# Kernel optimization log

Hardware: AMD Instinct MI355X
Metric: run time of the kernel (lower is better)

## Reference

```python
import jax, jax.numpy as jnp
import numpy as np

EPS = 1e-5
HEAD_SPLIT = 16   # MAB_new self.K: torch.split chunk size along channels (= head dim)
NUM_D = 16        # MAB_new self.d: becomes the number of heads; attn scale = 1/sqrt(d)


def _fc(x, W, b, g, be):
    # conv2d_ with 1x1 kernel acting on last dim + BatchNorm2d (training-mode
    # batch statistics over B,T,N per channel) + ReLU.  x: [B,T,N,Cin]
    y = jnp.einsum('btnc,oc->btno', x, W) + b
    mu = y.mean(axis=(0, 1, 2), keepdims=True)
    var = y.var(axis=(0, 1, 2), keepdims=True)  # biased var, as torch BN
    return jax.nn.relu(g * (y - mu) * jax.lax.rsqrt(var + EPS) + be)


def _mab(Q, Kin, pq, pk, pv, po):
    q = _fc(Q, *pq)
    k = _fc(Kin, *pk)
    v = _fc(Kin, *pv)
    B, Sq, N, D = q.shape
    Sk = k.shape[1]
    h = D // HEAD_SPLIT  # = NUM_D heads of size HEAD_SPLIT (split/cat quirk)
    qh = q.reshape(B, Sq, N, h, HEAD_SPLIT)
    kh = k.reshape(B, Sk, N, h, HEAD_SPLIT)
    vh = v.reshape(B, Sk, N, h, HEAD_SPLIT)
    scale = np.float32(1.0 / np.sqrt(NUM_D))
    attn = jnp.einsum('bqnhc,bknhc->bnhqk', qh, kh) * scale
    attn = jax.nn.softmax(attn, axis=-1)
    out = jnp.einsum('bnhqk,bknhc->bqnhc', attn, vh).reshape(B, Sq, N, D)
    return _fc(out, *po)


def _forward(X, TE, SE, I,
             m0qW, m0qb, m0qg, m0qz, m0kW, m0kb, m0kg, m0kz,
             m0vW, m0vb, m0vg, m0vz, m0oW, m0ob, m0og, m0oz,
             m1qW, m1qb, m1qg, m1qz, m1kW, m1kb, m1kg, m1kz,
             m1vW, m1vb, m1vg, m1vz, m1oW, m1ob, m1og, m1oz):
    mid = X
    Xc = jnp.concatenate([X, TE, SE], axis=-1)           # [B,T,N,3D]
    Ir = jnp.broadcast_to(I, (X.shape[0],) + I.shape[1:])  # [B,set_dim,N,3D]
    H = _mab(Ir, Xc, (m0qW, m0qb, m0qg, m0qz), (m0kW, m0kb, m0kg, m0kz),
             (m0vW, m0vb, m0vg, m0vz), (m0oW, m0ob, m0og, m0oz))
    res = _mab(Xc, H, (m1qW, m1qb, m1qg, m1qz), (m1kW, m1kb, m1kg, m1kz),
               (m1vW, m1vb, m1vg, m1vz), (m1oW, m1ob, m1og, m1oz))
    return mid + res


def setup_inputs() -> dict:
    key = jax.random.key(0)
    ks = list(jax.random.split(key, 64))
    B, T, N, D = 16, 12, 500, 256
    DD, S = 3 * D, 32
    nxt = iter(ks)

    def w(o, i):
        return jax.random.normal(next(nxt), (o, i), jnp.float32) * np.float32(1.0 / np.sqrt(i))

    inp = {
        'X': jax.random.normal(next(nxt), (B, T, N, D), jnp.float32),
        'TE': jax.random.normal(next(nxt), (B, T, N, D), jnp.float32),
        'SE': jax.random.normal(next(nxt), (B, T, N, D), jnp.float32),
        'I': jax.random.normal(next(nxt), (1, S, N, DD), jnp.float32) * np.float32(0.02),
    }
    layer_shapes = {'m0': [('q', D, DD), ('k', D, DD), ('v', D, DD), ('o', DD, D)],
                    'm1': [('q', D, DD), ('k', D, DD), ('v', D, DD), ('o', D, D)]}
    for pre in ('m0', 'm1'):
        for name, o, i in layer_shapes[pre]:
            inp[pre + name + 'W'] = w(o, i)
            inp[pre + name + 'b'] = jnp.zeros((o,), jnp.float32)
            inp[pre + name + 'g'] = jax.random.uniform(next(nxt), (o,), jnp.float32, 0.5, 1.5)
            inp[pre + name + 'z'] = jax.random.normal(next(nxt), (o,), jnp.float32) * np.float32(0.1)
    inp['mask'] = jnp.ones((1,), jnp.bool_)  # unused in original forward
    return inp


def reference(X, TE, SE, I,
              m0qW, m0qb, m0qg, m0qz, m0kW, m0kb, m0kg, m0kz,
              m0vW, m0vb, m0vg, m0vz, m0oW, m0ob, m0og, m0oz,
              m1qW, m1qb, m1qg, m1qz, m1kW, m1kb, m1kg, m1kz,
              m1vW, m1vb, m1vg, m1vz, m1oW, m1ob, m1og, m1oz, mask):
    return _forward(X, TE, SE, I,
                    m0qW, m0qb, m0qg, m0qz, m0kW, m0kb, m0kg, m0kz,
                    m0vW, m0vb, m0vg, m0vz, m0oW, m0ob, m0og, m0oz,
                    m1qW, m1qb, m1qg, m1qz, m1kW, m1kb, m1kg, m1kz,
                    m1vW, m1vb, m1vg, m1vz, m1oW, m1ob, m1og, m1oz)
```

## Files before the change

kernel.cpp:

```cpp
#include <hip/hip_runtime.h>
#include <stdint.h>

typedef __bf16 bf16_t;
typedef bf16_t bf16x8 __attribute__((ext_vector_type(8)));
typedef float f32x4 __attribute__((ext_vector_type(4)));

__device__ __forceinline__ float bf2f(unsigned short u) {
  union { unsigned int i; float f; } x; x.i = ((unsigned int)u) << 16; return x.f;
}
__device__ __forceinline__ unsigned short f2bf(float f) {
  union { float f; unsigned int i; } x; x.f = f;
  unsigned int r = x.i + 0x7FFFu + ((x.i >> 16) & 1u);
  return (unsigned short)(r >> 16);
}
__device__ __forceinline__ unsigned pack2(float a, float b) {
  return (unsigned)f2bf(a) | ((unsigned)f2bf(b) << 16);
}

__global__ void cat3(const float* __restrict__ a, const float* __restrict__ b,
                     const float* __restrict__ c, float* __restrict__ dst) {
  int i = threadIdx.x;
  dst[i] = a[i]; dst[256 + i] = b[i]; dst[512 + i] = c[i];
}

__global__ __launch_bounds__(256) void wsplit(
    const float* __restrict__ in, unsigned short* __restrict__ hi,
    unsigned short* __restrict__ lo, int n) {
  int i = (blockIdx.x * 256 + threadIdx.x) * 8;
  if (i >= n) return;
  float4 a = *(const float4*)(in + i);
  float4 b = *(const float4*)(in + i + 4);
  float f[8] = {a.x, a.y, a.z, a.w, b.x, b.y, b.z, b.w};
  unsigned short sh[8], sl[8];
#pragma unroll
  for (int j = 0; j < 8; ++j) {
    sh[j] = f2bf(f[j]);
    sl[j] = f2bf(f[j] - bf2f(sh[j]));
  }
  *(uint4*)(hi + i) = *(uint4*)sh;
  *(uint4*)(lo + i) = *(uint4*)sl;
}

struct f8 { float4 a, b; };

__device__ __forceinline__ f8 ld_c8(const float* __restrict__ X,
                                    const float* __restrict__ TE,
                                    const float* __restrict__ SE,
                                    size_t row, int cc) {
  const float* src = (cc < 256) ? X : ((cc < 512) ? TE : SE);
  const float* p = src + row * 256 + (cc & 255);
  f8 r; r.a = *(const float4*)p; r.b = *(const float4*)(p + 4);
  return r;
}
__device__ __forceinline__ uint4 pack_hi(const float4 a, const float4 b) {
  return make_uint4(pack2(a.x, a.y), pack2(a.z, a.w), pack2(b.x, b.y), pack2(b.z, b.w));
}

template<int AMODE, int SMODE, int PART, int PREC, int K>
__global__ __launch_bounds__(512) void gemm7(
    const void* __restrict__ Ap, const float* __restrict__ AX,
    const float* __restrict__ ATE, const float* __restrict__ ASE,
    const unsigned short* __restrict__ Wh, const unsigned short* __restrict__ Wl,
    const float* __restrict__ bias, const float2* __restrict__ ssO,
    unsigned short* __restrict__ Cb, unsigned short* __restrict__ Cb2,
    float* __restrict__ psum, float* __restrict__ psq,
    int Cout, int cstr, int pOff, int nx) {
  constexpr int ASH = 64 * K;
  constexpr int TOT = ASH + (SMODE != 0 ? 64 * 136 : 8);
  constexpr int NC = K / 128;
  __shared__ unsigned short lds[TOT];
  unsigned short* lA = lds;
  unsigned short* lC = lds + ASH;

  const int tid = threadIdx.x;
  const int lane = tid & 63, wid = tid >> 6;
  const int l15 = lane & 15, l4 = lane >> 4;
  const int brow = blockIdx.x * 64;

  constexpr int CPR = K / 8;
#pragma unroll
  for (int i = 0; i < (64 * CPR) / 512; ++i) {
    int ch = i * 512 + tid;
    int row = ch / CPR, c8 = (ch % CPR) * 8;
    uint4 hv;
    if constexpr (AMODE == 2) {
      hv = *(const uint4*)((const unsigned short*)Ap + (size_t)(brow + row) * K + c8);
    } else if constexpr (AMODE == 0) {
      const float* p = (const float*)Ap + (size_t)(brow + row) * K + c8;
      hv = pack_hi(*(const float4*)p, *(const float4*)(p + 4));
    } else {
      f8 v = ld_c8(AX, ATE, ASE, (size_t)(brow + row), c8);
      hv = pack_hi(v.a, v.b);
    }
    int dst = row * K + (c8 & ~63) + ((c8 & 63) ^ ((row & 7) << 3));
    *(uint4*)(lA + dst) = hv;
  }
  __syncthreads();

  const int axor = (l15 & 7) << 3;
  const int colL = wid * 16 + l15;

  for (int cx = 0; cx < nx; ++cx) {
    const int bcol = cx * 256;
    const bool lo0 = (PREC == 2) || (PREC == 3 && bcol >= 256);
    const bool lo1 = (PREC == 2) || (PREC == 3 && bcol + 128 >= 256);
    const unsigned short* wH0 = Wh + (size_t)(bcol + colL) * K + l4 * 8;
    const unsigned short* wH1 = wH0 + (size_t)128 * K;
    const unsigned short* wL0 = nullptr;
    const unsigned short* wL1 = nullptr;
    if constexpr (PREC >= 2) {
      wL0 = Wl + (size_t)(bcol + colL) * K + l4 * 8;
      wL1 = wL0 + (size_t)128 * K;
    }
    f32x4 acc[4][2] = {};

#pragma unroll
    for (int c = 0; c < NC; ++c) {
      uint4 bh0[4], bh1[4], bl0[4], bl1[4];
#pragma unroll
      for (int ks = 0; ks < 4; ++ks) {
        bh0[ks] = *(const uint4*)(wH0 + c * 128 + ks * 32);
        bh1[ks] = *(const uint4*)(wH1 + c * 128 + ks * 32);
      }
      if constexpr (PREC >= 2) {
        if (lo0) {
#pragma unroll
          for (int ks = 0; ks < 4; ++ks) bl0[ks] = *(const uint4*)(wL0 + c * 128 + ks * 32);
        }
        if (lo1) {
#pragma unroll
          for (int ks = 0; ks < 4; ++ks) bl1[ks] = *(const uint4*)(wL1 + c * 128 + ks * 32);
        }
      }
#pragma unroll
      for (int kk = 0; kk < 4; ++kk) {
        const int kabs = c * 128 + kk * 32;
        const int kt64 = kabs & ~63;
        const int cofs = ((kabs & 32) + l4 * 8) ^ axor;
        bf16x8 af[4];
#pragma unroll
        for (int m = 0; m < 4; ++m)
          af[m] = *(const bf16x8*)(lA + (m * 16 + l15) * K + kt64 + cofs);
        bf16x8 b0 = *(const bf16x8*)&bh0[kk];
        bf16x8 b1 = *(const bf16x8*)&bh1[kk];
#pragma unroll
        for (int m = 0; m < 4; ++m) {
          acc[m][0] = __builtin_amdgcn_mfma_f32_16x16x32_bf16(af[m], b0, acc[m][0], 0, 0, 0);
          acc[m][1] = __builtin_amdgcn_mfma_f32_16x16x32_bf16(af[m], b1, acc[m][1], 0, 0, 0);
        }
        if constexpr (PREC >= 2) {
          if (lo0) {
            bf16x8 c0 = *(const bf16x8*)&bl0[kk];
#pragma unroll
            for (int m = 0; m < 4; ++m)
              acc[m][0] = __builtin_amdgcn_mfma_f32_16x16x32_bf16(af[m], c0, acc[m][0], 0, 0, 0);
          }
          if (lo1) {
            bf16x8 c1 = *(const bf16x8*)&bl1[kk];
#pragma unroll
            for (int m = 0; m < 4; ++m)
              acc[m][1] = __builtin_amdgcn_mfma_f32_16x16x32_bf16(af[m], c1, acc[m][1], 0, 0, 0);
          }
        }
      }
    }

#pragma unroll
    for (int s = 0; s < 2; ++s) {
      const int bcs = bcol + s * 128;
      const int col = bcs + colL;
      float cs = 0.f, cq = 0.f;
      float bv = bias[col];
      float2 s2 = make_float2(1.f, 0.f);
      if constexpr (SMODE == 2) s2 = ssO[col];
      if constexpr (SMODE != 0) __syncthreads();
#pragma unroll
      for (int m = 0; m < 4; ++m) {
#pragma unroll
        for (int r = 0; r < 4; ++r) {
          float v = acc[m][s][r] + bv;
          if constexpr (PART) { cs += v; cq += v * v; }
          if constexpr (SMODE == 2) v = fmaxf(v * s2.x + s2.y, 0.f);
          if constexpr (SMODE != 0) lC[(m * 16 + l4 * 4 + r) * 136 + colL] = f2bf(v);
        }
      }
      if constexpr (SMODE != 0) {
        __syncthreads();
        const int rw = tid >> 4, c16 = (tid & 15) * 8;
#pragma unroll
        for (int it = 0; it < 2; ++it) {
          int rr = it * 32 + rw;
          uint4 val = *(const uint4*)(lC + rr * 136 + c16);
          if constexpr (SMODE == 5) {
            unsigned short* dst = (bcs < 256) ? Cb : Cb2;
            *(uint4*)(dst + (size_t)(brow + rr) * 256 + (bcs & 255) + c16) = val;
          } else if constexpr (SMODE == 6) {
            if (bcs < 512)
              *(uint4*)(Cb + (size_t)(brow + rr) * 512 + bcs + c16) = val;
            else
              *(uint4*)(Cb2 + (size_t)(brow + rr) * 256 + (bcs - 512) + c16) = val;
          } else {
            *(uint4*)(Cb + (size_t)(brow + rr) * cstr + bcs + c16) = val;
          }
        }
      }
      if constexpr (PART) {
        cs += __shfl_xor(cs, 16); cs += __shfl_xor(cs, 32);
        cq += __shfl_xor(cq, 16); cq += __shfl_xor(cq, 32);
        if (l4 == 0) {
          size_t pidx = (size_t)(pOff + blockIdx.x) * Cout + col;
          psum[pidx] = cs;
          psq[pidx]  = cq;
        }
      }
    }
  }
}

__global__ __launch_bounds__(256) void colstats(
    const unsigned short* __restrict__ A, float* __restrict__ psum,
    float* __restrict__ psq) {
  const int tid = threadIdx.x;
  const int r8 = tid >> 5, co = tid & 31;
  float s[8] = {0,0,0,0,0,0,0,0}, q[8] = {0,0,0,0,0,0,0,0};
  size_t base = (size_t)blockIdx.x * 2048;
  for (int it = 0; it < 256; ++it) {
    size_t row = base + it * 8 + r8;
    uint4 v = *(const uint4*)(A + row * 256 + co * 8);
    const unsigned short* pv = (const unsigned short*)&v;
#pragma unroll
    for (int j = 0; j < 8; ++j) {
      float f = bf2f(pv[j]);
      s[j] += f; q[j] += f * f;
    }
  }
  __shared__ float ls[8][32][8], lq[8][32][8];
#pragma unroll
  for (int j = 0; j < 8; ++j) { ls[r8][co][j] = s[j]; lq[r8][co][j] = q[j]; }
  __syncthreads();
  int co2 = tid >> 3, j2 = tid & 7;
  float S = 0.f, Q = 0.f;
#pragma unroll
  for (int r = 0; r < 8; ++r) { S += ls[r][co2][j2]; Q += lq[r][co2][j2]; }
  psum[(size_t)blockIdx.x * 256 + co2 * 8 + j2] = S;
  psq [(size_t)blockIdx.x * 256 + co2 * 8 + j2] = Q;
}

__global__ __launch_bounds__(512) void bn_part(
    const float* __restrict__ psum, const float* __restrict__ psq,
    float* __restrict__ pp, int gridM, int Cout) {
  const int lane = threadIdx.x & 63, wv = threadIdx.x >> 6;
  const int c = blockIdx.y * 64 + lane;
  float s = 0.f, q = 0.f;
  for (int r = blockIdx.x + 64 * wv; r < gridM; r += 512) {
    s += psum[(size_t)r * Cout + c];
    q += psq[(size_t)r * Cout + c];
  }
  __shared__ float rs[8][64], rq[8][64];
  rs[wv][lane] = s; rq[wv][lane] = q;
  __syncthreads();
  if (threadIdx.x < 64) {
    float S = 0.f, Q = 0.f;
#pragma unroll
    for (int w2 = 0; w2 < 8; ++w2) { S += rs[w2][threadIdx.x]; Q += rq[w2][threadIdx.x]; }
    pp[(size_t)blockIdx.x * Cout + blockIdx.y * 64 + threadIdx.x] = S;
    pp[(size_t)(64 + blockIdx.x) * Cout + blockIdx.y * 64 + threadIdx.x] = Q;
  }
}
__global__ __launch_bounds__(64) void bn_fin(
    const float* __restrict__ pp, const float* __restrict__ g,
    const float* __restrict__ be, float2* __restrict__ ss,
    int CoutT, int colOff, float invR) {
  int c = blockIdx.x * 64 + threadIdx.x;
  int cp = colOff + c;
  float S = 0.f, Q = 0.f;
  for (int r = 0; r < 64; ++r) {
    S += pp[(size_t)r * CoutT + cp];
    Q += pp[(size_t)(64 + r) * CoutT + cp];
  }
  float mu = S * invR, var = Q * invR - mu * mu;
  float sc = g[c] * rsqrtf(var + 1e-5f);
  ss[c] = make_float2(sc, be[c] - mu * sc);
}
__global__ __launch_bounds__(64) void bn_fin2(
    const float* __restrict__ pp, const float* __restrict__ gA,
    const float* __restrict__ zA, const float* __restrict__ gB,
    const float* __restrict__ zB, float2* __restrict__ ssC,
    int CoutT, float invR) {
  int c = blockIdx.x * 64 + threadIdx.x;
  float S = 0.f, Q = 0.f;
  for (int r = 0; r < 64; ++r) {
    S += pp[(size_t)r * CoutT + c];
    Q += pp[(size_t)(64 + r) * CoutT + c];
  }
  float mu = S * invR, var = Q * invR - mu * mu;
  const float* g = (c < 256) ? gA : gB;
  const float* z = (c < 256) ? zA : zB;
  int ci = c & 255;
  float sc = g[ci] * rsqrtf(var + 1e-5f);
  ssC[c] = make_float2(sc, z[ci] - mu * sc);
}

template<int NK, int NQ>
__global__ void attn_sm(const unsigned short* __restrict__ qy,
                        const unsigned short* __restrict__ ky,
                        const unsigned short* __restrict__ vy,
                        const float2* __restrict__ ssq, const float2* __restrict__ ssk,
                        const float2* __restrict__ ssv, unsigned short* __restrict__ out,
                        size_t qStride, size_t kvStride, size_t oStride, int RS) {
  __shared__ float kl[NK][16][17];
  __shared__ float vl[NK][16][17];
  const int n = blockIdx.x, b = blockIdx.y;
  const int tid = threadIdx.x;
  const unsigned short* kyb = ky + (size_t)b * kvStride;
  const unsigned short* vyb = vy + (size_t)b * kvStride;
  for (int ch = tid; ch < NK * 32; ch += NQ * 16) {
    int t = ch >> 5, c8 = (ch & 31) * 8;
    size_t src = ((size_t)t * 500 + n) * RS + c8;
    uint4 kv = *(const uint4*)(kyb + src);
    uint4 vv = *(const uint4*)(vyb + src);
    const unsigned short* kp = (const unsigned short*)&kv;
    const unsigned short* vp = (const unsigned short*)&vv;
#pragma unroll
    for (int j = 0; j < 8; ++j) {
      int c = c8 + j;
      float2 sk = ssk[c], sv = ssv[c];
      kl[t][c >> 4][c & 15] = fmaxf(bf2f(kp[j]) * sk.x + sk.y, 0.f);
      vl[t][c >> 4][c & 15] = fmaxf(bf2f(vp[j]) * sv.x + sv.y, 0.f);
    }
  }
  __syncthreads();
  const int s = tid >> 4, h = tid & 15;
  unsigned short qraw[16];
  size_t qb = (size_t)b * qStride + ((size_t)s * 500 + n) * 256 + h * 16;
  *(uint4*)qraw = *(const uint4*)(qy + qb);
  *(uint4*)(qraw + 8) = *(const uint4*)(qy + qb + 8);
  float qv[16];
#pragma unroll
  for (int c = 0; c < 16; ++c) {
    float2 sq = ssq[h * 16 + c];
    qv[c] = fmaxf(bf2f(qraw[c]) * sq.x + sq.y, 0.f);
  }
  float lg[NK], mx = -1e30f;
#pragma unroll
  for (int t = 0; t < NK; ++t) {
    float d = 0.f;
#pragma unroll
    for (int c = 0; c < 16; ++c) d += qv[c] * kl[t][h][c];
    lg[t] = d * 0.25f;
    mx = fmaxf(mx, lg[t]);
  }
  float sum = 0.f;
#pragma unroll
  for (int t = 0; t < NK; ++t) { lg[t] = __expf(lg[t] - mx); sum += lg[t]; }
  float inv = 1.f / sum;
  float o[16];
#pragma unroll
  for (int c = 0; c < 16; ++c) o[c] = 0.f;
#pragma unroll
  for (int t = 0; t < NK; ++t) {
    float p = lg[t] * inv;
#pragma unroll
    for (int c = 0; c < 16; ++c) o[c] += p * vl[t][h][c];
  }
  size_t ob = (size_t)b * oStride + ((size_t)s * 500 + n) * 256 + h * 16;
  uint4 w0;
  w0.x = pack2(o[0], o[1]); w0.y = pack2(o[2], o[3]);
  w0.z = pack2(o[4], o[5]); w0.w = pack2(o[6], o[7]);
  *(uint4*)(out + ob) = w0;
  w0.x = pack2(o[8], o[9]); w0.y = pack2(o[10], o[11]);
  w0.z = pack2(o[12], o[13]); w0.w = pack2(o[14], o[15]);
  *(uint4*)(out + ob + 8) = w0;
}

__global__ __launch_bounds__(256) void bn_relu_addx(
    const unsigned short* __restrict__ y, const float2* __restrict__ ss,
    const float* __restrict__ X, float* __restrict__ out) {
  int r = blockIdx.x * 8 + (threadIdx.x >> 5);
  int c8 = (threadIdx.x & 31) * 8;
  size_t idx = (size_t)r * 256 + c8;
  uint4 yv4 = *(const uint4*)(y + idx);
  const unsigned short* yv = (const unsigned short*)&yv4;
  float4 x0 = *(const float4*)(X + idx);
  float4 x1 = *(const float4*)(X + idx + 4);
  float ov[8];
#pragma unroll
  for (int j = 0; j < 8; ++j) {
    float2 sc = ss[c8 + j];
    ov[j] = fmaxf(bf2f(yv[j]) * sc.x + sc.y, 0.f);
  }
  *(float4*)(out + idx)     = make_float4(x0.x + ov[0], x0.y + ov[1], x0.z + ov[2], x0.w + ov[3]);
  *(float4*)(out + idx + 4) = make_float4(x1.x + ov[4], x1.y + ov[5], x1.z + ov[6], x1.w + ov[7]);
}

extern "C" void kernel_launch(void* const* d_in, const int* in_sizes, int n_in,
                              void* d_out, int out_size, void* d_ws, size_t ws_size,
                              hipStream_t stream) {
  (void)in_sizes; (void)n_in; (void)out_size; (void)ws_size;
  const float* X  = (const float*)d_in[0];
  const float* TE = (const float*)d_in[1];
  const float* SE = (const float*)d_in[2];
  const float* I  = (const float*)d_in[3];
  const float *Wf[8], *Bf[8], *Gf[8], *Zf[8];
  for (int l = 0; l < 8; ++l) {
    Wf[l] = (const float*)d_in[4 + l * 4 + 0];
    Bf[l] = (const float*)d_in[4 + l * 4 + 1];
    Gf[l] = (const float*)d_in[4 + l * 4 + 2];
    Zf[l] = (const float*)d_in[4 + l * 4 + 3];
  }

  char* w = (char*)d_ws;
  size_t off = 0;
  auto alloc = [&](size_t bytes) -> void* {
    void* p = w + off;
    off += (bytes + 255) & ~(size_t)255;
    return p;
  };

  float* psum0 = (float*)alloc((size_t)4000 * 768 * 4);
  float* psq0  = (float*)alloc((size_t)4000 * 768 * 4);
  float* psumK = (float*)alloc((size_t)125 * 256 * 4);
  float* psqK  = (float*)alloc((size_t)125 * 256 * 4);
  float* pp    = (float*)alloc((size_t)128 * 768 * 4);
  float2* ss   = (float2*)alloc((size_t)(8 * 768 + 512) * sizeof(float2));
  float2* ssC  = ss + 8 * 768;
  unsigned short *W0h, *W0l, *W3h, *W3l, *W7h, *W7l;
  unsigned short *KVQh, *KVQl, *KV1h, *KV1l;
  W0h = (unsigned short*)alloc(196608 * 2); W0l = (unsigned short*)alloc(196608 * 2);
  W3h = (unsigned short*)alloc(196608 * 2); W3l = (unsigned short*)alloc(196608 * 2);
  W7h = (unsigned short*)alloc(65536 * 2);  W7l = (unsigned short*)alloc(65536 * 2);
  KVQh = (unsigned short*)alloc(589824 * 2); KVQl = (unsigned short*)alloc(589824 * 2);
  KV1h = (unsigned short*)alloc(393216 * 2); KV1l = (unsigned short*)alloc(393216 * 2);
  float* b124 = (float*)alloc(768 * 4);
  float* b56  = (float*)alloc(512 * 4);
  char* R = (char*)alloc(131072000);
  unsigned short* q0  = (unsigned short*)R;
  unsigned short* kv0 = (unsigned short*)(R + 8192000);
  unsigned short* k1  = (unsigned short*)R;
  unsigned short* o0b = (unsigned short*)alloc(131072000);
  unsigned short* v1  = o0b;
  unsigned short* y7  = o0b;
  unsigned short* Hc  = (unsigned short*)alloc((size_t)32000 * 768 * 2);

  unsigned short* q1 = (unsigned short*)d_out;
  unsigned short* o1 = (unsigned short*)d_out + 24576000;

  cat3<<<dim3(1), 256, 0, stream>>>(Bf[1], Bf[2], Bf[4], b124);
  cat3<<<dim3(1), 256, 0, stream>>>(Bf[5], Bf[6], Bf[6], b56);
  wsplit<<<dim3(96), 256, 0, stream>>>(Wf[0], W0h, W0l, 196608);
  wsplit<<<dim3(96), 256, 0, stream>>>(Wf[3], W3h, W3l, 196608);
  wsplit<<<dim3(32), 256, 0, stream>>>(Wf[7], W7h, W7l, 65536);
  wsplit<<<dim3(96), 256, 0, stream>>>(Wf[1], KVQh, KVQl, 196608);
  wsplit<<<dim3(96), 256, 0, stream>>>(Wf[2], KVQh + 196608, KVQl + 196608, 196608);
  wsplit<<<dim3(96), 256, 0, stream>>>(Wf[4], KVQh + 393216, KVQl + 393216, 196608);
  wsplit<<<dim3(96), 256, 0, stream>>>(Wf[5], KV1h, KV1l, 196608);
  wsplit<<<dim3(96), 256, 0, stream>>>(Wf[6], KV1h + 196608, KV1l + 196608, 196608);

  auto bn1 = [&](float* ps, float* pq, const float* g, const float* z, float2* dst,
                 int gridM, int Cout, float invR) {
    bn_part<<<dim3(64, Cout / 64), 512, 0, stream>>>(ps, pq, pp, gridM, Cout);
    bn_fin<<<dim3(Cout / 64), 64, 0, stream>>>(pp, g, z, dst, Cout, 0, invR);
  };

  gemm7<0, 1, 1, 2, 768><<<dim3(250), 512, 0, stream>>>(
      I, nullptr, nullptr, nullptr, W0h, W0l, Bf[0], nullptr,
      q0, nullptr, psum0, psq0, 256, 256, 0, 1);
  bn1(psum0, psq0, Gf[0], Zf[0], ss + 0 * 768, 250, 256, 1.f / 16000.f);
  gemm7<1, 6, 1, 2, 768><<<dim3(1500), 512, 0, stream>>>(
      nullptr, X, TE, SE, KVQh, KVQl, b124, nullptr,
      kv0, q1, psum0, psq0, 768, 0, 0, 3);
  bn_part<<<dim3(64, 12), 512, 0, stream>>>(psum0, psq0, pp, 1500, 768);
  bn_fin2<<<dim3(8), 64, 0, stream>>>(pp, Gf[1], Zf[1], Gf[2], Zf[2], ssC, 768, 1.f / 96000.f);
  bn_fin<<<dim3(4), 64, 0, stream>>>(pp, Gf[4], Zf[4], ss + 4 * 768, 768, 512, 1.f / 96000.f);

  attn_sm<12, 32><<<dim3(500, 16), 512, 0, stream>>>(
      q0, kv0, kv0 + 256, ss + 0 * 768, ssC, ssC + 256, o0b,
      0, (size_t)6000 * 512, (size_t)16000 * 256, 512);

  gemm7<2, 0, 1, 1, 256><<<dim3(4000), 512, 0, stream>>>(
      o0b, nullptr, nullptr, nullptr, W3h, W3l, Bf[3], nullptr,
      nullptr, nullptr, psum0, psq0, 768, 768, 0, 3);
  bn1(psum0, psq0, Gf[3], Zf[3], ss + 3 * 768, 4000, 768, 1.f / 256000.f);

  for (int cb = 0; cb < 8; ++cb) {
    const size_t oCh = (size_t)cb * 32000 * 256;
    gemm7<2, 2, 0, 2, 256><<<dim3(500), 512, 0, stream>>>(
        o0b + oCh, nullptr, nullptr, nullptr, W3h, W3l, Bf[3], ss + 3 * 768,
        Hc, nullptr, nullptr, nullptr, 768, 768, 0, 3);
    gemm7<2, 5, 0, 3, 768><<<dim3(500), 512, 0, stream>>>(
        Hc, nullptr, nullptr, nullptr, KV1h, KV1l, b56, nullptr,
        k1 + oCh, v1 + oCh, nullptr, nullptr, 512, 256, 0, 2);
  }

  colstats<<<dim3(125), 256, 0, stream>>>(k1, psumK, psqK);
  bn1(psumK, psqK, Gf[5], Zf[5], ss + 5 * 768, 125, 256, 1.f / 256000.f);
  colstats<<<dim3(125), 256, 0, stream>>>(v1, psumK, psqK);
  bn1(psumK, psqK, Gf[6], Zf[6], ss + 6 * 768, 125, 256, 1.f / 256000.f);

  attn_sm<32, 12><<<dim3(500, 16), 192, 0, stream>>>(
      q1, k1, v1, ss + 4 * 768, ss + 5 * 768, ss + 6 * 768, o1,
      (size_t)6000 * 256, (size_t)16000 * 256, (size_t)6000 * 256, 256);

  gemm7<2, 1, 1, 2, 256><<<dim3(1500), 512, 0, stream>>>(
      o1, nullptr, nullptr, nullptr, W7h, W7l, Bf[7], nullptr,
      y7, nullptr, psum0, psq0, 256, 256, 0, 1);
  bn1(psum0, psq0, Gf[7], Zf[7], ss + 7 * 768, 1500, 256, 1.f / 96000.f);
  bn_relu_addx<<<dim3(12000), 256, 0, stream>>>(y7, ss + 7 * 768, X, (float*)d_out);
}
```

Measured before the change: 2.504 ms.

## Add LDS-free bf16 GEMM reading A fragments directly from global memory

```diff
diff --git a/kernel.cpp b/kernel.cpp
--- a/kernel.cpp
+++ b/kernel.cpp
@@ -102,8 +102,9 @@
 
   for (int cx = 0; cx < nx; ++cx) {
     const int bcol = cx * 256;
-    const bool lo0 = (PREC == 2) || (PREC == 3 && bcol >= 256);
-    const bool lo1 = (PREC == 2) || (PREC == 3 && bcol + 128 >= 256);
+    const int bcs0 = bcol, bcs1 = bcol + 128;
+    const bool lo0 = (PREC == 2) || (PREC == 4 && bcs0 >= 256 && bcs0 < 512);
+    const bool lo1 = (PREC == 2) || (PREC == 4 && bcs1 >= 256 && bcs1 < 512);
     const unsigned short* wH0 = Wh + (size_t)(bcol + colL) * K + l4 * 8;
     const unsigned short* wH1 = wH0 + (size_t)128 * K;
     const unsigned short* wL0 = nullptr;
@@ -191,14 +192,142 @@
         for (int it = 0; it < 2; ++it) {
           int rr = it * 32 + rw;
           uint4 val = *(const uint4*)(lC + rr * 136 + c16);
-          if constexpr (SMODE == 5) {
-            unsigned short* dst = (bcs < 256) ? Cb : Cb2;
-            *(uint4*)(dst + (size_t)(brow + rr) * 256 + (bcs & 255) + c16) = val;
-          } else if constexpr (SMODE == 6) {
+          if constexpr (SMODE == 6) {
             if (bcs < 512)
               *(uint4*)(Cb + (size_t)(brow + rr) * 512 + bcs + c16) = val;
             else
               *(uint4*)(Cb2 + (size_t)(brow + rr) * 256 + (bcs - 512) + c16) = val;
+          } else {
+            *(uint4*)(Cb + (size_t)(brow + rr) * cstr + bcs + c16) = val;
+          }
+        }
+      }
+      if constexpr (PART) {
+        cs += __shfl_xor(cs, 16); cs += __shfl_xor(cs, 32);
+        cq += __shfl_xor(cq, 16); cq += __shfl_xor(cq, 32);
+        if (l4 == 0) {
+          size_t pidx = (size_t)(pOff + blockIdx.x) * Cout + col;
+          psum[pidx] = cs;
+          psq[pidx]  = cq;
+        }
+      }
+    }
+  }
+}
+
+template<int SMODE, int PART, int PREC, int K>
+__global__ __launch_bounds__(512, 4) void gemm8(
+    const unsigned short* __restrict__ A,
+    const unsigned short* __restrict__ Wh, const unsigned short* __restrict__ Wl,
+    const float* __restrict__ bias, const float2* __restrict__ ssO,
+    unsigned short* __restrict__ Cb, unsigned short* __restrict__ Cb2,
+    float* __restrict__ psum, float* __restrict__ psq,
+    int Cout, int cstr, int pOff, int nx) {
+  constexpr int TOT = (SMODE != 0) ? 64 * 136 : 8;
+  constexpr int NB = K / 64;
+  __shared__ unsigned short lC[TOT];
+
+  const int tid = threadIdx.x;
+  const int lane = tid & 63, wid = tid >> 6;
+  const int l15 = lane & 15, l4 = lane >> 4;
+  const int brow = blockIdx.x * 64;
+  const int colL = wid * 16 + l15;
+
+  const unsigned short* aBase = A + (size_t)(brow + l15) * K + l4 * 8;
+
+  for (int cx = 0; cx < nx; ++cx) {
+    const int bcol = cx * 256;
+    const int bcs0 = bcol, bcs1 = bcol + 128;
+    const bool lo0 = (PREC == 2) || (PREC == 3 && bcs0 >= 256);
+    const bool lo1 = (PREC == 2) || (PREC == 3 && bcs1 >= 256);
+    const unsigned short* wH0 = Wh + (size_t)(bcol + colL) * K + l4 * 8;
+    const unsigned short* wH1 = wH0 + (size_t)128 * K;
+    const unsigned short* wL0 = nullptr;
+    const unsigned short* wL1 = nullptr;
+    if constexpr (PREC >= 2) {
+      wL0 = Wl + (size_t)(bcol + colL) * K + l4 * 8;
+      wL1 = wL0 + (size_t)128 * K;
+    }
+    f32x4 acc[4][2] = {};
+
+#pragma unroll
+    for (int c = 0; c < NB; ++c) {
+      uint4 bh0[2], bh1[2], bl0[2], bl1[2];
+#pragma unroll
+      for (int ks = 0; ks < 2; ++ks) {
+        bh0[ks] = *(const uint4*)(wH0 + c * 64 + ks * 32);
+        bh1[ks] = *(const uint4*)(wH1 + c * 64 + ks * 32);
+      }
+      if constexpr (PREC >= 2) {
+        if (lo0) {
+#pragma unroll
+          for (int ks = 0; ks < 2; ++ks) bl0[ks] = *(const uint4*)(wL0 + c * 64 + ks * 32);
+        }
+        if (lo1) {
+#pragma unroll
+          for (int ks = 0; ks < 2; ++ks) bl1[ks] = *(const uint4*)(wL1 + c * 64 + ks * 32);
+        }
+      }
+#pragma unroll
+      for (int kk = 0; kk < 2; ++kk) {
+        const int kabs = c * 64 + kk * 32;
+        bf16x8 af[4];
+#pragma unroll
+        for (int m = 0; m < 4; ++m)
+          af[m] = *(const bf16x8*)(aBase + (size_t)(m * 16) * K + kabs);
+        bf16x8 b0 = *(const bf16x8*)&bh0[kk];
+        bf16x8 b1 = *(const bf16x8*)&bh1[kk];
+#pragma unroll
+        for (int m = 0; m < 4; ++m) {
+          acc[m][0] = __builtin_amdgcn_mfma_f32_16x16x32_bf16(af[m], b0, acc[m][0], 0, 0, 0);
+          acc[m][1] = __builtin_amdgcn_mfma_f32_16x16x32_bf16(af[m], b1, acc[m][1], 0, 0, 0);
+        }
+        if constexpr (PREC >= 2) {
+          if (lo0) {
+            bf16x8 c0 = *(const bf16x8*)&bl0[kk];
+#pragma unroll
+            for (int m = 0; m < 4; ++m)
+              acc[m][0] = __builtin_amdgcn_mfma_f32_16x16x32_bf16(af[m], c0, acc[m][0], 0, 0, 0);
+          }
+          if (lo1) {
+            bf16x8 c1 = *(const bf16x8*)&bl1[kk];
+#pragma unroll
+            for (int m = 0; m < 4; ++m)
+              acc[m][1] = __builtin_amdgcn_mfma_f32_16x16x32_bf16(af[m], c1, acc[m][1], 0, 0, 0);
+          }
+        }
+      }
+    }
+
+#pragma unroll
+    for (int s = 0; s < 2; ++s) {
+      const int bcs = bcol + s * 128;
+      const int col = bcs + colL;
+      float cs = 0.f, cq = 0.f;
+      float bv = bias[col];
+      float2 s2 = make_float2(1.f, 0.f);
+      if constexpr (SMODE == 2) s2 = ssO[col];
+      if constexpr (SMODE != 0) __syncthreads();
+#pragma unroll
+      for (int m = 0; m < 4; ++m) {
+#pragma unroll
+        for (int r = 0; r < 4; ++r) {
+          float v = acc[m][s][r] + bv;
+          if constexpr (PART) { cs += v; cq += v * v; }
+          if constexpr (SMODE == 2) v = fmaxf(v * s2.x + s2.y, 0.f);
+          if constexpr (SMODE != 0) lC[(m * 16 + l4 * 4 + r) * 136 + colL] = f2bf(v);
+        }
+      }
+      if constexpr (SMODE != 0) {
+        __syncthreads();
+        const int rw = tid >> 4, c16 = (tid & 15) * 8;
+#pragma unroll
+        for (int it = 0; it < 2; ++it) {
+          int rr = it * 32 + rw;
+          uint4 val = *(const uint4*)(lC + rr * 136 + c16);
+          if constexpr (SMODE == 5) {
+            unsigned short* dst = (bcs < 256) ? Cb : Cb2;
+            *(uint4*)(dst + (size_t)(brow + rr) * 256 + (bcs & 255) + c16) = val;
           } else {
             *(uint4*)(Cb + (size_t)(brow + rr) * cstr + bcs + c16) = val;
           }
@@ -466,7 +595,7 @@
       I, nullptr, nullptr, nullptr, W0h, W0l, Bf[0], nullptr,
       q0, nullptr, psum0, psq0, 256, 256, 0, 1);
   bn1(psum0, psq0, Gf[0], Zf[0], ss + 0 * 768, 250, 256, 1.f / 16000.f);
-  gemm7<1, 6, 1, 2, 768><<<dim3(1500), 512, 0, stream>>>(
+  gemm7<1, 6, 1, 4, 768><<<dim3(1500), 512, 0, stream>>>(
       nullptr, X, TE, SE, KVQh, KVQl, b124, nullptr,
       kv0, q1, psum0, psq0, 768, 0, 0, 3);
   bn_part<<<dim3(64, 12), 512, 0, stream>>>(psum0, psq0, pp, 1500, 768);
@@ -477,19 +606,19 @@
       q0, kv0, kv0 + 256, ss + 0 * 768, ssC, ssC + 256, o0b,
       0, (size_t)6000 * 512, (size_t)16000 * 256, 512);
 
-  gemm7<2, 0, 1, 1, 256><<<dim3(4000), 512, 0, stream>>>(
-      o0b, nullptr, nullptr, nullptr, W3h, W3l, Bf[3], nullptr,
-      nullptr, nullptr, psum0, psq0, 768, 768, 0, 3);
+  gemm8<0, 1, 1, 256><<<dim3(4000), 512, 0, stream>>>(
+      o0b, W3h, W3l, Bf[3], nullptr, nullptr, nullptr,
+      psum0, psq0, 768, 768, 0, 3);
   bn1(psum0, psq0, Gf[3], Zf[3], ss + 3 * 768, 4000, 768, 1.f / 256000.f);
 
   for (int cb = 0; cb < 8; ++cb) {
     const size_t oCh = (size_t)cb * 32000 * 256;
-    gemm7<2, 2, 0, 2, 256><<<dim3(500), 512, 0, stream>>>(
-        o0b + oCh, nullptr, nullptr, nullptr, W3h, W3l, Bf[3], ss + 3 * 768,
-        Hc, nullptr, nullptr, nullptr, 768, 768, 0, 3);
-    gemm7<2, 5, 0, 3, 768><<<dim3(500), 512, 0, stream>>>(
-        Hc, nullptr, nullptr, nullptr, KV1h, KV1l, b56, nullptr,
-        k1 + oCh, v1 + oCh, nullptr, nullptr, 512, 256, 0, 2);
+    gemm8<2, 0, 2, 256><<<dim3(500), 512, 0, stream>>>(
+        o0b + oCh, W3h, W3l, Bf[3], ss + 3 * 768, Hc, nullptr,
+        nullptr, nullptr, 768, 768, 0, 3);
+    gemm8<5, 0, 3, 768><<<dim3(500), 512, 0, stream>>>(
+        Hc, KV1h, KV1l, b56, nullptr, k1 + oCh, v1 + oCh,
+        nullptr, nullptr, 512, 256, 0, 2);
   }
 
   colstats<<<dim3(125), 256, 0, stream>>>(k1, psumK, psqK);
@@ -501,9 +630,9 @@
       q1, k1, v1, ss + 4 * 768, ss + 5 * 768, ss + 6 * 768, o1,
       (size_t)6000 * 256, (size_t)16000 * 256, (size_t)6000 * 256, 256);
 
-  gemm7<2, 1, 1, 2, 256><<<dim3(1500), 512, 0, stream>>>(
-      o1, nullptr, nullptr, nullptr, W7h, W7l, Bf[7], nullptr,
-      y7, nullptr, psum0, psq0, 256, 256, 0, 1);
+  gemm8<1, 1, 2, 256><<<dim3(1500), 512, 0, stream>>>(
+      o1, W7h, W7l, Bf[7], nullptr, y7, nullptr,
+      psum0, psq0, 256, 256, 0, 1);
   bn1(psum0, psq0, Gf[7], Zf[7], ss + 7 * 768, 1500, 256, 1.f / 96000.f);
   bn_relu_addx<<<dim3(12000), 256, 0, stream>>>(y7, ss + 7 * 768, X, (float*)d_out);
 }
```

Result: slower. 4.828 ms (+92.8%).

## Parameterize GEMM row tile and add mixed-precision mode for fused QKV projection

Applied to the files above, without the earlier changes.

```diff
diff --git a/kernel.cpp b/kernel.cpp
--- a/kernel.cpp
+++ b/kernel.cpp
@@ -56,7 +56,7 @@
   return make_uint4(pack2(a.x, a.y), pack2(a.z, a.w), pack2(b.x, b.y), pack2(b.z, b.w));
 }
 
-template<int AMODE, int SMODE, int PART, int PREC, int K>
+template<int AMODE, int SMODE, int PART, int PREC, int K, int BM>
 __global__ __launch_bounds__(512) void gemm7(
     const void* __restrict__ Ap, const float* __restrict__ AX,
     const float* __restrict__ ATE, const float* __restrict__ ASE,
@@ -65,9 +65,10 @@
     unsigned short* __restrict__ Cb, unsigned short* __restrict__ Cb2,
     float* __restrict__ psum, float* __restrict__ psq,
     int Cout, int cstr, int pOff, int nx) {
-  constexpr int ASH = 64 * K;
-  constexpr int TOT = ASH + (SMODE != 0 ? 64 * 136 : 8);
+  constexpr int ASH = BM * K;
+  constexpr int TOT = ASH + (SMODE != 0 ? BM * 136 : 8);
   constexpr int NC = K / 128;
+  constexpr int MR = BM / 16;
   __shared__ unsigned short lds[TOT];
   unsigned short* lA = lds;
   unsigned short* lC = lds + ASH;
@@ -75,11 +76,11 @@
   const int tid = threadIdx.x;
   const int lane = tid & 63, wid = tid >> 6;
   const int l15 = lane & 15, l4 = lane >> 4;
-  const int brow = blockIdx.x * 64;
+  const int brow = blockIdx.x * BM;
 
   constexpr int CPR = K / 8;
 #pragma unroll
-  for (int i = 0; i < (64 * CPR) / 512; ++i) {
+  for (int i = 0; i < (BM * CPR) / 512; ++i) {
     int ch = i * 512 + tid;
     int row = ch / CPR, c8 = (ch % CPR) * 8;
     uint4 hv;
@@ -102,8 +103,11 @@
 
   for (int cx = 0; cx < nx; ++cx) {
     const int bcol = cx * 256;
-    const bool lo0 = (PREC == 2) || (PREC == 3 && bcol >= 256);
-    const bool lo1 = (PREC == 2) || (PREC == 3 && bcol + 128 >= 256);
+    const int bcs0 = bcol, bcs1 = bcol + 128;
+    const bool lo0 = (PREC == 2) || (PREC == 3 && bcs0 >= 256) ||
+                     (PREC == 4 && bcs0 >= 256 && bcs0 < 512);
+    const bool lo1 = (PREC == 2) || (PREC == 3 && bcs1 >= 256) ||
+                     (PREC == 4 && bcs1 >= 256 && bcs1 < 512);
     const unsigned short* wH0 = Wh + (size_t)(bcol + colL) * K + l4 * 8;
     const unsigned short* wH1 = wH0 + (size_t)128 * K;
     const unsigned short* wL0 = nullptr;
@@ -112,7 +116,7 @@
       wL0 = Wl + (size_t)(bcol + colL) * K + l4 * 8;
       wL1 = wL0 + (size_t)128 * K;
     }
-    f32x4 acc[4][2] = {};
+    f32x4 acc[MR][2] = {};
 
 #pragma unroll
     for (int c = 0; c < NC; ++c) {
@@ -137,14 +141,14 @@
         const int kabs = c * 128 + kk * 32;
         const int kt64 = kabs & ~63;
         const int cofs = ((kabs & 32) + l4 * 8) ^ axor;
-        bf16x8 af[4];
-#pragma unroll
-        for (int m = 0; m < 4; ++m)
+        bf16x8 af[MR];
+#pragma unroll
+        for (int m = 0; m < MR; ++m)
           af[m] = *(const bf16x8*)(lA + (m * 16 + l15) * K + kt64 + cofs);
         bf16x8 b0 = *(const bf16x8*)&bh0[kk];
         bf16x8 b1 = *(const bf16x8*)&bh1[kk];
 #pragma unroll
-        for (int m = 0; m < 4; ++m) {
+        for (int m = 0; m < MR; ++m) {
           acc[m][0] = __builtin_amdgcn_mfma_f32_16x16x32_bf16(af[m], b0, acc[m][0], 0, 0, 0);
           acc[m][1] = __builtin_amdgcn_mfma_f32_16x16x32_bf16(af[m], b1, acc[m][1], 0, 0, 0);
         }
@@ -152,13 +156,13 @@
           if (lo0) {
             bf16x8 c0 = *(const bf16x8*)&bl0[kk];
 #pragma unroll
-            for (int m = 0; m < 4; ++m)
+            for (int m = 0; m < MR; ++m)
               acc[m][0] = __builtin_amdgcn_mfma_f32_16x16x32_bf16(af[m], c0, acc[m][0], 0, 0, 0);
           }
           if (lo1) {
             bf16x8 c1 = *(const bf16x8*)&bl1[kk];
 #pragma unroll
-            for (int m = 0; m < 4; ++m)
+            for (int m = 0; m < MR; ++m)
               acc[m][1] = __builtin_amdgcn_mfma_f32_16x16x32_bf16(af[m], c1, acc[m][1], 0, 0, 0);
           }
         }
@@ -175,7 +179,7 @@
       if constexpr (SMODE == 2) s2 = ssO[col];
       if constexpr (SMODE != 0) __syncthreads();
 #pragma unroll
-      for (int m = 0; m < 4; ++m) {
+      for (int m = 0; m < MR; ++m) {
 #pragma unroll
         for (int r = 0; r < 4; ++r) {
           float v = acc[m][s][r] + bv;
@@ -188,7 +192,7 @@
         __syncthreads();
         const int rw = tid >> 4, c16 = (tid & 15) * 8;
 #pragma unroll
-        for (int it = 0; it < 2; ++it) {
+        for (int it = 0; it < BM / 32; ++it) {
           int rr = it * 32 + rw;
           uint4 val = *(const uint4*)(lC + rr * 136 + c16);
           if constexpr (SMODE == 5) {
@@ -462,14 +466,14 @@
     bn_fin<<<dim3(Cout / 64), 64, 0, stream>>>(pp, g, z, dst, Cout, 0, invR);
   };
 
-  gemm7<0, 1, 1, 2, 768><<<dim3(250), 512, 0, stream>>>(
+  gemm7<0, 1, 1, 2, 768, 32><<<dim3(500), 512, 0, stream>>>(
       I, nullptr, nullptr, nullptr, W0h, W0l, Bf[0], nullptr,
       q0, nullptr, psum0, psq0, 256, 256, 0, 1);
-  bn1(psum0, psq0, Gf[0], Zf[0], ss + 0 * 768, 250, 256, 1.f / 16000.f);
-  gemm7<1, 6, 1, 2, 768><<<dim3(1500), 512, 0, stream>>>(
+  bn1(psum0, psq0, Gf[0], Zf[0], ss + 0 * 768, 500, 256, 1.f / 16000.f);
+  gemm7<1, 6, 1, 4, 768, 32><<<dim3(3000), 512, 0, stream>>>(
       nullptr, X, TE, SE, KVQh, KVQl, b124, nullptr,
       kv0, q1, psum0, psq0, 768, 0, 0, 3);
-  bn_part<<<dim3(64, 12), 512, 0, stream>>>(psum0, psq0, pp, 1500, 768);
+  bn_part<<<dim3(64, 12), 512, 0, stream>>>(psum0, psq0, pp, 3000, 768);
   bn_fin2<<<dim3(8), 64, 0, stream>>>(pp, Gf[1], Zf[1], Gf[2], Zf[2], ssC, 768, 1.f / 96000.f);
   bn_fin<<<dim3(4), 64, 0, stream>>>(pp, Gf[4], Zf[4], ss + 4 * 768, 768, 512, 1.f / 96000.f);
 
@@ -477,17 +481,17 @@
       q0, kv0, kv0 + 256, ss + 0 * 768, ssC, ssC + 256, o0b,
       0, (size_t)6000 * 512, (size_t)16000 * 256, 512);
 
-  gemm7<2, 0, 1, 1, 256><<<dim3(4000), 512, 0, stream>>>(
+  gemm7<2, 0, 1, 1, 256, 64><<<dim3(4000), 512, 0, stream>>>(
       o0b, nullptr, nullptr, nullptr, W3h, W3l, Bf[3], nullptr,
       nullptr, nullptr, psum0, psq0, 768, 768, 0, 3);
   bn1(psum0, psq0, Gf[3], Zf[3], ss + 3 * 768, 4000, 768, 1.f / 256000.f);
 
   for (int cb = 0; cb < 8; ++cb) {
     const size_t oCh = (size_t)cb * 32000 * 256;
-    gemm7<2, 2, 0, 2, 256><<<dim3(500), 512, 0, stream>>>(
+    gemm7<2, 2, 0, 2, 256, 64><<<dim3(500), 512, 0, stream>>>(
         o0b + oCh, nullptr, nullptr, nullptr, W3h, W3l, Bf[3], ss + 3 * 768,
         Hc, nullptr, nullptr, nullptr, 768, 768, 0, 3);
-    gemm7<2, 5, 0, 3, 768><<<dim3(500), 512, 0, stream>>>(
+    gemm7<2, 5, 0, 3, 768, 32><<<dim3(1000), 512, 0, stream>>>(
         Hc, nullptr, nullptr, nullptr, KV1h, KV1l, b56, nullptr,
         k1 + oCh, v1 + oCh, nullptr, nullptr, 512, 256, 0, 2);
   }
@@ -501,7 +505,7 @@
       q1, k1, v1, ss + 4 * 768, ss + 5 * 768, ss + 6 * 768, o1,
       (size_t)6000 * 256, (size_t)16000 * 256, (size_t)6000 * 256, 256);
 
-  gemm7<2, 1, 1, 2, 256><<<dim3(1500), 512, 0, stream>>>(
+  gemm7<2, 1, 1, 2, 256, 64><<<dim3(1500), 512, 0, stream>>>(
       o1, nullptr, nullptr, nullptr, W7h, W7l, Bf[7], nullptr,
       y7, nullptr, psum0, psq0, 256, 256, 0, 1);
   bn1(psum0, psq0, Gf[7], Zf[7], ss + 7 * 768, 1500, 256, 1.f / 96000.f);
```

After: 3.052 ms, median of 4. +21.9%, slower.
